# Optimization experiments

Hardware: AMD Instinct MI355X
Metric: run time of the kernel (lower is better)

## Reference

```python
import jax, jax.numpy as jnp
import numpy as np

N_NODES = 50000
D = 128
E_RAND = 640000
ALPHA = 0.2  # LeakyReLU negative slope


def setup_inputs() -> dict:
    key = jax.random.key(0)
    k1, k2, k3, k4, k5 = jax.random.split(key, 5)
    inputs = jax.random.normal(k1, (N_NODES, D), dtype=jnp.float32) * 0.1
    # xavier_normal with gain=1.414 as in the torch module
    W = jax.random.normal(k2, (D, D), dtype=jnp.float32) * (1.414 * np.sqrt(2.0 / (D + D)))
    a = jax.random.normal(k3, (2 * D,), dtype=jnp.float32) * (1.414 * np.sqrt(2.0 / (1 + 2 * D)))
    # random edges + self-loops so every node has at least one outgoing edge (nonzero rowsum)
    src = jnp.concatenate([jax.random.randint(k4, (E_RAND,), 0, N_NODES), jnp.arange(N_NODES)])
    dst = jnp.concatenate([jax.random.randint(k5, (E_RAND,), 0, N_NODES), jnp.arange(N_NODES)])
    edge = jnp.stack([src, dst]).astype(jnp.int64)
    return {"inputs": inputs, "edge": edge, "W": W, "a": a}


def reference(inputs, edge, W, a):
    N = inputs.shape[0]
    src, dst = edge[0], edge[1]
    h = inputs @ W  # [N, D]
    # a @ [h_src; h_dst] per edge == h_src @ a[:D] + h_dst @ a[D:]
    score = h[src] @ a[:D] + h[dst] @ a[D:]  # [E]
    edge_e = jnp.exp(jax.nn.leaky_relu(score, negative_slope=ALPHA))  # [E]
    # sparse.mm(coo(edge, edge_e), ones): rowsum over src (coalesce sums duplicates)
    e_rowsum = jax.ops.segment_sum(edge_e, src, num_segments=N)  # [N]
    # sparse.mm(coo(edge, edge_e), h): weighted aggregation of h[dst] into src rows
    h_prime = jax.ops.segment_sum(edge_e[:, None] * h[dst], src, num_segments=N)  # [N, D]
    h_prime = h_prime / e_rowsum[:, None]
    return jax.nn.elu(h_prime)
```

## Files before the change

kernel.cpp:

```cpp
#include <hip/hip_runtime.h>
#include <hip/hip_bf16.h>


constexpr int D   = 128;
constexpr int CH  = 4096;
constexpr int CAP = 4608;

typedef __attribute__((ext_vector_type(8))) short bf16x8;
typedef __attribute__((ext_vector_type(4))) float f32x4;

__device__ __forceinline__ short f2bf(float f) {
    unsigned u = __float_as_uint(f);
    unsigned r = (u + 0x7fffu + ((u >> 16) & 1u)) >> 16;
    return (short)r;
}
__device__ __forceinline__ float bf2f(short b) {
    return __uint_as_float(((unsigned)(unsigned short)b) << 16);
}
__device__ __forceinline__ short2 pk_bf16(float x, float y) {
    __hip_bfloat162 bb = __float22bfloat162_rn(make_float2(x, y));
    short2 r;
    __builtin_memcpy(&r, &bb, 4);
    return r;
}

__global__ __launch_bounds__(256) void prep_and_count(
    const float* __restrict__ W, short* __restrict__ bw,
    const int* __restrict__ src, int* __restrict__ cell_start,
    int* __restrict__ bucket_cnt, int NBK, int NC, int E) {
    __shared__ int hist[256];
    if (blockIdx.x >= (unsigned)NC) {
        const int tid = (blockIdx.x - NC) * 256 + threadIdx.x;
        const int l = tid & 63, st = tid >> 6;
        const int s = st >> 3, t = st & 7;
        const int n = t * 16 + (l & 15);
        const int q = l >> 4;
#pragma unroll
        for (int j = 0; j < 8; ++j) {
            const int k = s * 32 + q * 8 + j;
            bw[tid * 8 + j] = f2bf(W[k * D + n]);
        }
        return;
    }
    const int c = blockIdx.x, t = threadIdx.x;
    hist[t] = 0;
    __syncthreads();
    const int lo = c * CH, hi = min(lo + CH, E);
    const int hi4 = lo + ((hi - lo) & ~3);
    for (int i = lo + t * 4; i < hi4; i += 1024) {
        const int4 s4 = *(const int4*)(src + i);
        atomicAdd(&hist[s4.x >> 8], 1);
        atomicAdd(&hist[s4.y >> 8], 1);
        atomicAdd(&hist[s4.z >> 8], 1);
        atomicAdd(&hist[s4.w >> 8], 1);
    }
    for (int i = hi4 + t; i < hi; i += 256)
        atomicAdd(&hist[src[i] >> 8], 1);
    __syncthreads();
    for (int b = t; b < NBK; b += 256)
        cell_start[b * NC + c] = atomicAdd(&bucket_cnt[b], hist[b]);
}

__global__ __launch_bounds__(256) void gemm_and_binscatter(
    const float* __restrict__ X, const short* __restrict__ bw,
    const float* __restrict__ a, short* __restrict__ h,
    float* __restrict__ s1, float* __restrict__ s2,
    const int* __restrict__ src, const int* __restrict__ dst,
    const int* __restrict__ cell_start, int* __restrict__ binned,
    int NBK, int NC, int N, int E) {
    __shared__ int cnt[256];
    if (blockIdx.x < (unsigned)NC) {
        const int c = blockIdx.x, t = threadIdx.x;
        cnt[t] = 0;
        __syncthreads();
        const int lo = c * CH, hi = min(lo + CH, E);
        const int hi4 = lo + ((hi - lo) & ~3);
        for (int i = lo + t * 4; i < hi4; i += 1024) {
            const int4 s4 = *(const int4*)(src + i);
            const int4 d4 = *(const int4*)(dst + i);
            const int sv[4] = {s4.x, s4.y, s4.z, s4.w};
            const int dv[4] = {d4.x, d4.y, d4.z, d4.w};
#pragma unroll
            for (int j = 0; j < 4; ++j) {
                const int b = sv[j] >> 8;
                const int r = atomicAdd(&cnt[b], 1);
                binned[b * CAP + cell_start[b * NC + c] + r] =
                    ((sv[j] & 255) << 16) | dv[j];
            }
        }
        for (int i = hi4 + t; i < hi; i += 256) {
            const int s = src[i];
            const int b = s >> 8;
            const int r = atomicAdd(&cnt[b], 1);
            binned[b * CAP + cell_start[b * NC + c] + r] = ((s & 255) << 16) | dst[i];
        }
        return;
    }
    const int wave = threadIdx.x >> 6, lane = threadIdx.x & 63;
    const int r0 = (blockIdx.x - NC) * 64 + wave * 16;
    const int m = lane & 15, q = lane >> 4;
    const int arow = r0 + m;
    const bool rowok = arow < N;
    const float* xp = X + (size_t)arow * D + q * 8;

    f32x4 acc[8] = {};
#pragma unroll
    for (int s = 0; s < 4; ++s) {
        float4 xa = {0, 0, 0, 0}, xb = {0, 0, 0, 0};
        if (rowok) {
            xa = *(const float4*)(xp + s * 32);
            xb = *(const float4*)(xp + s * 32 + 4);
        }
        bf16x8 af;
        short2 c0 = pk_bf16(xa.x, xa.y), c1 = pk_bf16(xa.z, xa.w);
        short2 c2 = pk_bf16(xb.x, xb.y), c3 = pk_bf16(xb.z, xb.w);
        af[0] = c0.x; af[1] = c0.y; af[2] = c1.x; af[3] = c1.y;
        af[4] = c2.x; af[5] = c2.y; af[6] = c3.x; af[7] = c3.y;
#pragma unroll
        for (int t = 0; t < 8; ++t) {
            bf16x8 bf = *(const bf16x8*)(bw + ((s * 8 + t) * 64 + lane) * 8);
            acc[t] = __builtin_amdgcn_mfma_f32_16x16x32_bf16(af, bf, acc[t], 0, 0, 0);
        }
    }
    float a1v[8], a2v[8];
#pragma unroll
    for (int t = 0; t < 8; ++t) {
        a1v[t] = a[t * 16 + m];
        a2v[t] = a[D + t * 16 + m];
    }
    float p1[4] = {0, 0, 0, 0}, p2[4] = {0, 0, 0, 0};
#pragma unroll
    for (int t = 0; t < 8; ++t) {
        short2 h01 = pk_bf16(acc[t][0], acc[t][1]);
        short2 h23 = pk_bf16(acc[t][2], acc[t][3]);
        const short hb[4] = {h01.x, h01.y, h23.x, h23.y};
#pragma unroll
        for (int i = 0; i < 4; ++i) {
            const int row = r0 + q * 4 + i;
            if (row < N) h[(size_t)row * D + t * 16 + m] = hb[i];
            const float hr = bf2f(hb[i]);
            p1[i] += hr * a1v[t];
            p2[i] += hr * a2v[t];
        }
    }
#pragma unroll
    for (int off = 1; off < 16; off <<= 1) {
#pragma unroll
        for (int i = 0; i < 4; ++i) {
            p1[i] += __shfl_xor(p1[i], off);
            p2[i] += __shfl_xor(p2[i], off);
        }
    }
    if (m < 4) {
        const int row = r0 + q * 4 + m;
        if (row < N) {
            const float v1 = (m == 0) ? p1[0] : (m == 1) ? p1[1] : (m == 2) ? p1[2] : p1[3];
            const float v2 = (m == 0) ? p2[0] : (m == 1) ? p2[1] : (m == 2) ? p2[2] : p2[3];
            s1[row] = v1;
            s2[row] = v2;
        }
    }
}

__global__ __launch_bounds__(256) void fine_scatter(
    const int* __restrict__ binned, const int* __restrict__ bucket_cnt,
    int2* __restrict__ bounds, int* __restrict__ csrd, int N) {
    __shared__ int ncnt[256], snc[256], exclp[256], pcnt[256];
    const int b = blockIdx.x, t = threadIdx.x;
    ncnt[t] = 0;
    pcnt[t] = 0;
    __syncthreads();
    const int start = b * CAP;
    const int end = start + bucket_cnt[b];
    for (int i = start + t; i < end; i += 256)
        atomicAdd(&ncnt[binned[i] >> 16], 1);
    __syncthreads();
    snc[t] = ncnt[t];
    __syncthreads();
    for (int off = 1; off < 256; off <<= 1) {
        int v = (t >= off) ? snc[t - off] : 0;
        __syncthreads();
        snc[t] += v;
        __syncthreads();
    }
    exclp[t] = snc[t] - ncnt[t];
    const int node = b * 256 + t;
    if (node < N) bounds[node] = make_int2(start + exclp[t], start + exclp[t] + ncnt[t]);
    __syncthreads();
    for (int i = start + t; i < end; i += 256) {
        const int e = binned[i];
        const int r = e >> 16;
        csrd[start + exclp[r] + atomicAdd(&pcnt[r], 1)] = e & 0xFFFF;
    }
}

__global__ __launch_bounds__(256) void aggregate(
    const int* __restrict__ csrd, const int2* __restrict__ bounds,
    const float* __restrict__ s1, const float* __restrict__ s2,
    const short* __restrict__ h, float* __restrict__ out, int N) {
    const int n    = blockIdx.x * 4 + (threadIdx.x >> 6);
    const int lane = threadIdx.x & 63;
    if (n >= N) return;
    const int g = lane >> 4, m = lane & 15;
    const int2 be = bounds[n];
    const int beg = be.x, end = be.y;
    const float s1n = s1[n];

    int dA1 = csrd[min(beg + g, end - 1)];
    int dB1 = csrd[min(beg + 4 + g, end - 1)];
    float  sA0 = s2[dA1], sB0 = s2[dB1];
    bf16x8 rA0 = *(const bf16x8*)(h + (size_t)dA1 * D + m * 8);
    bf16x8 rB0 = *(const bf16x8*)(h + (size_t)dB1 * D + m * 8);
    dA1 = csrd[min(beg + 8 + g, end - 1)];
    dB1 = csrd[min(beg + 12 + g, end - 1)];

    float acc[8] = {};
    float rs = 0.f;
    for (int k0 = beg; k0 < end; k0 += 8) {
        const float  sA1 = s2[dA1];
        const float  sB1 = s2[dB1];
        const bf16x8 rA1 = *(const bf16x8*)(h + (size_t)dA1 * D + m * 8);
        const bf16x8 rB1 = *(const bf16x8*)(h + (size_t)dB1 * D + m * 8);
        dA1 = csrd[min(k0 + 16 + g, end - 1)];
        dB1 = csrd[min(k0 + 20 + g, end - 1)];

        float scA = s1n + sA0;
        scA = scA > 0.f ? scA : 0.2f * scA;
        float eA = __expf(scA);
        if (k0 + g >= end) eA = 0.f;
        float scB = s1n + sB0;
        scB = scB > 0.f ? scB : 0.2f * scB;
        float eB = __expf(scB);
        if (k0 + 4 + g >= end) eB = 0.f;
#pragma unroll
        for (int j = 0; j < 8; ++j)
            acc[j] += eA * bf2f(rA0[j]) + eB * bf2f(rB0[j]);
        rs += eA + eB;
        sA0 = sA1; sB0 = sB1; rA0 = rA1; rB0 = rB1;
    }
#pragma unroll
    for (int off = 16; off <= 32; off <<= 1) {
        rs += __shfl_xor(rs, off);
#pragma unroll
        for (int j = 0; j < 8; ++j) acc[j] += __shfl_xor(acc[j], off);
    }
    if (g == 0) {
        const float inv = 1.f / rs;
        float o[8];
#pragma unroll
        for (int j = 0; j < 8; ++j) {
            float v = acc[j] * inv;
            o[j] = v > 0.f ? v : expm1f(v);
        }
        float* op = out + (size_t)n * D + m * 8;
        *(float4*)op       = make_float4(o[0], o[1], o[2], o[3]);
        *(float4*)(op + 4) = make_float4(o[4], o[5], o[6], o[7]);
    }
}

extern "C" void kernel_launch(void* const* d_in, const int* in_sizes, int n_in,
                              void* d_out, int out_size, void* d_ws, size_t ws_size,
                              hipStream_t stream) {
    const float* X    = (const float*)d_in[0];
    const int*   edge = (const int*)d_in[1];
    const float* W    = (const float*)d_in[2];
    const float* a    = (const float*)d_in[3];
    float* out = (float*)d_out;

    const int N = in_sizes[0] / D;
    const int E = in_sizes[1] / 2;
    const int* src = edge;
    const int* dst = edge + E;

    const int NBK = (N + 255) >> 8;
    const int NC  = (E + CH - 1) / CH;
    const int cells = NBK * NC;
    const int NG  = (N + 63) / 64;

    char* ws = (char*)d_ws;
    short* h        = (short*)ws; ws += (size_t)N * D * sizeof(short);
    int* binned     = (int*)ws;   ws += (size_t)NBK * CAP * sizeof(int);
    int* csrd       = (int*)ws;   ws += (size_t)NBK * CAP * sizeof(int);
    short* bw       = (short*)ws; ws += 2048 * 8 * sizeof(short);
    float* s1       = (float*)ws; ws += (size_t)N * sizeof(float);
    float* s2       = (float*)ws; ws += (size_t)N * sizeof(float);
    int2* bounds    = (int2*)ws;  ws += (size_t)N * sizeof(int2);
    int* cell_start = (int*)ws;   ws += (size_t)cells * sizeof(int);
    int* bucket_cnt = (int*)ws;   ws += 256 * sizeof(int);

    (void)hipMemsetAsync(bucket_cnt, 0, NBK * sizeof(int), stream);
    prep_and_count<<<NC + 8, 256, 0, stream>>>(W, bw, src, cell_start, bucket_cnt,
                                               NBK, NC, E);
    gemm_and_binscatter<<<NC + NG, 256, 0, stream>>>(X, bw, a, h, s1, s2, src, dst,
                                                     cell_start, binned, NBK, NC, N, E);
    fine_scatter<<<NBK, 256, 0, stream>>>(binned, bucket_cnt, bounds, csrd, N);
    aggregate<<<(N + 3) / 4, 256, 0, stream>>>(csrd, bounds, s1, s2, h, out, N);
}
```

Before: 141.9 us.

## Merge histogram and bin-scatter into one kernel with per-block W conversion in LDS

```diff
diff --git a/kernel.cpp b/kernel.cpp
--- a/kernel.cpp
+++ b/kernel.cpp
@@ -3,7 +3,7 @@
 
 
 constexpr int D   = 128;
-constexpr int CH  = 4096;
+constexpr int CH  = 8192;
 constexpr int CAP = 4608;
 
 typedef __attribute__((ext_vector_type(8))) short bf16x8;
@@ -24,57 +24,35 @@
     return r;
 }
 
-__global__ __launch_bounds__(256) void prep_and_count(
-    const float* __restrict__ W, short* __restrict__ bw,
-    const int* __restrict__ src, int* __restrict__ cell_start,
-    int* __restrict__ bucket_cnt, int NBK, int NC, int E) {
-    __shared__ int hist[256];
-    if (blockIdx.x >= (unsigned)NC) {
-        const int tid = (blockIdx.x - NC) * 256 + threadIdx.x;
-        const int l = tid & 63, st = tid >> 6;
-        const int s = st >> 3, t = st & 7;
-        const int n = t * 16 + (l & 15);
-        const int q = l >> 4;
-#pragma unroll
-        for (int j = 0; j < 8; ++j) {
-            const int k = s * 32 + q * 8 + j;
-            bw[tid * 8 + j] = f2bf(W[k * D + n]);
-        }
-        return;
-    }
-    const int c = blockIdx.x, t = threadIdx.x;
-    hist[t] = 0;
-    __syncthreads();
-    const int lo = c * CH, hi = min(lo + CH, E);
-    const int hi4 = lo + ((hi - lo) & ~3);
-    for (int i = lo + t * 4; i < hi4; i += 1024) {
-        const int4 s4 = *(const int4*)(src + i);
-        atomicAdd(&hist[s4.x >> 8], 1);
-        atomicAdd(&hist[s4.y >> 8], 1);
-        atomicAdd(&hist[s4.z >> 8], 1);
-        atomicAdd(&hist[s4.w >> 8], 1);
-    }
-    for (int i = hi4 + t; i < hi; i += 256)
-        atomicAdd(&hist[src[i] >> 8], 1);
-    __syncthreads();
-    for (int b = t; b < NBK; b += 256)
-        cell_start[b * NC + c] = atomicAdd(&bucket_cnt[b], hist[b]);
-}
-
-__global__ __launch_bounds__(256) void gemm_and_binscatter(
-    const float* __restrict__ X, const short* __restrict__ bw,
-    const float* __restrict__ a, short* __restrict__ h,
-    float* __restrict__ s1, float* __restrict__ s2,
+__global__ __launch_bounds__(256) void sort_and_gemm(
+    const float* __restrict__ X, const float* __restrict__ W,
+    const float* __restrict__ a,
     const int* __restrict__ src, const int* __restrict__ dst,
-    const int* __restrict__ cell_start, int* __restrict__ binned,
+    int* __restrict__ bucket_cnt, int* __restrict__ binned,
+    short* __restrict__ h, float* __restrict__ s1, float* __restrict__ s2,
     int NBK, int NC, int N, int E) {
-    __shared__ int cnt[256];
+    __shared__ short lbw[2048 * 8];
     if (blockIdx.x < (unsigned)NC) {
+        int* hist = (int*)lbw;
+        int* base = hist + 256;
         const int c = blockIdx.x, t = threadIdx.x;
-        cnt[t] = 0;
+        hist[t] = 0;
         __syncthreads();
         const int lo = c * CH, hi = min(lo + CH, E);
         const int hi4 = lo + ((hi - lo) & ~3);
+        for (int i = lo + t * 4; i < hi4; i += 1024) {
+            const int4 s4 = *(const int4*)(src + i);
+            atomicAdd(&hist[s4.x >> 8], 1);
+            atomicAdd(&hist[s4.y >> 8], 1);
+            atomicAdd(&hist[s4.z >> 8], 1);
+            atomicAdd(&hist[s4.w >> 8], 1);
+        }
+        for (int i = hi4 + t; i < hi; i += 256)
+            atomicAdd(&hist[src[i] >> 8], 1);
+        __syncthreads();
+        if (t < NBK) base[t] = atomicAdd(&bucket_cnt[t], hist[t]);
+        hist[t] = 0;
+        __syncthreads();
         for (int i = lo + t * 4; i < hi4; i += 1024) {
             const int4 s4 = *(const int4*)(src + i);
             const int4 d4 = *(const int4*)(dst + i);
@@ -83,19 +61,29 @@
 #pragma unroll
             for (int j = 0; j < 4; ++j) {
                 const int b = sv[j] >> 8;
-                const int r = atomicAdd(&cnt[b], 1);
-                binned[b * CAP + cell_start[b * NC + c] + r] =
-                    ((sv[j] & 255) << 16) | dv[j];
+                const int r = atomicAdd(&hist[b], 1);
+                binned[b * CAP + base[b] + r] = ((sv[j] & 255) << 16) | dv[j];
             }
         }
         for (int i = hi4 + t; i < hi; i += 256) {
             const int s = src[i];
             const int b = s >> 8;
-            const int r = atomicAdd(&cnt[b], 1);
-            binned[b * CAP + cell_start[b * NC + c] + r] = ((s & 255) << 16) | dst[i];
+            const int r = atomicAdd(&hist[b], 1);
+            binned[b * CAP + base[b] + r] = ((s & 255) << 16) | dst[i];
         }
         return;
     }
+    for (int i = threadIdx.x; i < 2048; i += 256) {
+        const int l = i & 63, st = i >> 6;
+        const int s = st >> 3, tt = st & 7;
+        const int n = tt * 16 + (l & 15);
+        const int q = l >> 4;
+#pragma unroll
+        for (int j = 0; j < 8; ++j)
+            lbw[i * 8 + j] = f2bf(W[(s * 32 + q * 8 + j) * D + n]);
+    }
+    __syncthreads();
+
     const int wave = threadIdx.x >> 6, lane = threadIdx.x & 63;
     const int r0 = (blockIdx.x - NC) * 64 + wave * 16;
     const int m = lane & 15, q = lane >> 4;
@@ -118,7 +106,7 @@
         af[4] = c2.x; af[5] = c2.y; af[6] = c3.x; af[7] = c3.y;
 #pragma unroll
         for (int t = 0; t < 8; ++t) {
-            bf16x8 bf = *(const bf16x8*)(bw + ((s * 8 + t) * 64 + lane) * 8);
+            bf16x8 bf = *(const bf16x8*)(lbw + ((s * 8 + t) * 64 + lane) * 8);
             acc[t] = __builtin_amdgcn_mfma_f32_16x16x32_bf16(af, bf, acc[t], 0, 0, 0);
         }
     }
@@ -274,25 +262,20 @@
 
     const int NBK = (N + 255) >> 8;
     const int NC  = (E + CH - 1) / CH;
-    const int cells = NBK * NC;
     const int NG  = (N + 63) / 64;
 
     char* ws = (char*)d_ws;
     short* h        = (short*)ws; ws += (size_t)N * D * sizeof(short);
     int* binned     = (int*)ws;   ws += (size_t)NBK * CAP * sizeof(int);
     int* csrd       = (int*)ws;   ws += (size_t)NBK * CAP * sizeof(int);
-    short* bw       = (short*)ws; ws += 2048 * 8 * sizeof(short);
     float* s1       = (float*)ws; ws += (size_t)N * sizeof(float);
     float* s2       = (float*)ws; ws += (size_t)N * sizeof(float);
     int2* bounds    = (int2*)ws;  ws += (size_t)N * sizeof(int2);
-    int* cell_start = (int*)ws;   ws += (size_t)cells * sizeof(int);
     int* bucket_cnt = (int*)ws;   ws += 256 * sizeof(int);
 
     (void)hipMemsetAsync(bucket_cnt, 0, NBK * sizeof(int), stream);
-    prep_and_count<<<NC + 8, 256, 0, stream>>>(W, bw, src, cell_start, bucket_cnt,
-                                               NBK, NC, E);
-    gemm_and_binscatter<<<NC + NG, 256, 0, stream>>>(X, bw, a, h, s1, s2, src, dst,
-                                                     cell_start, binned, NBK, NC, N, E);
+    sort_and_gemm<<<NC + NG, 256, 0, stream>>>(X, W, a, src, dst, bucket_cnt,
+                                               binned, h, s1, s2, NBK, NC, N, E);
     fine_scatter<<<NBK, 256, 0, stream>>>(binned, bucket_cnt, bounds, csrd, N);
     aggregate<<<(N + 3) / 4, 256, 0, stream>>>(csrd, bounds, s1, s2, h, out, N);
 }
```

New measurement: 140.8 us. Within noise of the previous version (-0.8%).
